# Kernel tuning notes

Measured on AMD Instinct MI355X. Metric: run time of the kernel, lower is better.

The kernel has to match this reference:

```python
import jax, jax.numpy as jnp
import numpy as np

N, E, F_IN, H, C_OUT, G, L = 50000, 400000, 128, 128, 10, 512, 3
EPS = 1e-5
BN_BIAS = 1e-4  # BatchNorm1d weights init to 1, biases to 1e-4 in the source


def batchnorm(x):
    # training-mode BN, gamma=1, beta=1e-4 (as initialized in the module)
    m = x.mean(0)
    v = jnp.mean((x - m) ** 2, 0)
    return (x - m) * jax.lax.rsqrt(v + EPS) + BN_BIAS


def gcn_conv(x, W, b, src, dst, edge_weight=None):
    """CAL-style GCNConv: x@W, add self loops (weight 1), sym deg^-1/2 norm, scatter-add to dst."""
    n = x.shape[0]
    h = x @ W
    ew = jnp.ones(src.shape[0], x.dtype) if edge_weight is None else edge_weight
    loop = jnp.arange(n)
    row = jnp.concatenate([src, loop])
    col = jnp.concatenate([dst, loop])
    ew = jnp.concatenate([ew, jnp.ones(n, x.dtype)])
    deg = jax.ops.segment_sum(ew, row, num_segments=n)
    dis = jax.lax.rsqrt(jnp.where(deg > 0, deg, 1.0)) * (deg > 0)
    norm = dis[row] * ew * dis[col]
    out = jax.ops.segment_sum(norm[:, None] * h[row], col, num_segments=n)
    return out + b


def setup_inputs():
    key = jax.random.key(0)
    ks = jax.random.split(key, 32)
    rn = lambda k, shp, s=0.1: jax.random.normal(k, shp, jnp.float32) * s
    src = jax.random.randint(ks[0], (E,), 0, N, jnp.int32)
    dst = jax.random.randint(ks[1], (E,), 0, N, jnp.int32)
    dst = jnp.where(dst == src, (dst + 1) % N, dst)  # no self loops in data edges
    batch = jnp.sort(jax.random.randint(ks[2], (N,), 0, G, jnp.int32))
    return {
        'x': jax.random.normal(ks[3], (N, F_IN), jnp.float32),
        'W_feat': rn(ks[4], (F_IN, H)),
        'conv_Ws': rn(ks[5], (L, H, H)), 'conv_bs': rn(ks[6], (L, H), 0.01),
        'eW': rn(ks[7], (2 * H, 2)), 'eb': rn(ks[8], (2,), 0.01),
        'naW': rn(ks[9], (H, 2)), 'nab': rn(ks[10], (2,), 0.01),
        'xcW': rn(ks[11], (H, H)), 'xcb': rn(ks[12], (H,), 0.01),
        'xoW': rn(ks[13], (H, H)), 'xob': rn(ks[14], (H,), 0.01),
        'cW1': rn(ks[15], (H, H)), 'cb1': rn(ks[16], (H,), 0.01),
        'cW2': rn(ks[17], (H, C_OUT)), 'cb2': rn(ks[18], (C_OUT,), 0.01),
        'oW1': rn(ks[19], (H, H)), 'ob1': rn(ks[20], (H,), 0.01),
        'oW2': rn(ks[21], (H, C_OUT)), 'ob2': rn(ks[22], (C_OUT,), 0.01),
        'coW1': rn(ks[23], (2 * H, H)), 'cob1': rn(ks[24], (H,), 0.01),
        'coW2': rn(ks[25], (H, C_OUT)), 'cob2': rn(ks[26], (C_OUT,), 0.01),
        'edge_src': src, 'edge_dst': dst, 'batch': batch,
    }


def _forward(x, W_feat, conv_Ws, conv_bs, eW, eb, naW, nab, xcW, xcb, xoW, xob,
             cW1, cb1, cW2, cb2, oW1, ob1, oW2, ob2, coW1, cob1, coW2, cob2,
             edge_src, edge_dst, batch):
    # BIG: BN -> gfn conv (linear, no bias, no propagate) -> [BN -> GCNConv -> relu] x L
    h = batchnorm(x)
    h = jax.nn.relu(h @ W_feat)
    for i in range(L):
        h = batchnorm(h)
        h = jax.nn.relu(gcn_conv(h, conv_Ws[i], conv_bs[i], edge_src, edge_dst))
    # Att_cov: per-edge MLP softmax + per-node GCNConv softmax (shared by XC/XO)
    edge_rep = jnp.concatenate([h[edge_src], h[edge_dst]], axis=-1)  # [E, 2H]
    edge_att = jax.nn.softmax(edge_rep @ eW + eb, axis=-1)           # [E, 2]
    node_att = jax.nn.softmax(gcn_conv(h, naW, nab, edge_src, edge_dst), axis=-1)  # [N, 2]
    # XC branch (channel 0)
    xc = node_att[:, 0:1] * h
    xc = jax.nn.elu(gcn_conv(batchnorm(xc), xcW, xcb, edge_src, edge_dst, edge_att[:, 0]))
    xc = jax.ops.segment_sum(xc, batch, num_segments=G)  # global_add_pool [G, H]
    # XO branch (channel 1)
    xo = node_att[:, 1:2] * h
    xo = jax.nn.elu(gcn_conv(batchnorm(xo), xoW, xob, edge_src, edge_dst, edge_att[:, 1]))
    xo = jax.ops.segment_sum(xo, batch, num_segments=G)
    # C head
    c = batchnorm(xc)
    c = jax.nn.relu(c @ cW1 + cb1)
    c = batchnorm(c)
    c = jax.nn.log_softmax(c @ cW2 + cb2, axis=-1)
    # O head (Dropout1d inactive in eval)
    o = batchnorm(xo)
    o = jax.nn.relu(o @ oW1 + ob1)
    o = batchnorm(o)
    o = jax.nn.log_softmax(o @ oW2 + ob2, axis=-1)
    # CO head (cat branch; eval_random=False -> identity permutation); note elu applied twice
    co = jnp.concatenate([xc, xo], axis=1)
    co = batchnorm(co)
    co = jax.nn.elu(jax.nn.elu(co @ coW1 + cob1))
    co = batchnorm(co)
    co = jax.nn.log_softmax(co @ coW2 + cob2, axis=-1)
    return c, o, co


def reference(x, W_feat, conv_Ws, conv_bs, eW, eb, naW, nab, xcW, xcb, xoW, xob,
              cW1, cb1, cW2, cb2, oW1, ob1, oW2, ob2, coW1, cob1, coW2, cob2,
              edge_src, edge_dst, batch):
    return _forward(x, W_feat, conv_Ws, conv_bs, eW, eb, naW, nab, xcW, xcb, xoW, xob,
                    cW1, cb1, cW2, cb2, oW1, ob1, oW2, ob2, coW1, cob1, coW2, cob2,
                    edge_src, edge_dst, batch)
```

## Files before the change

### kernel.cpp

```cpp
#include <hip/hip_runtime.h>


typedef unsigned short bf16_t;
typedef unsigned int   uint32;
typedef __attribute__((ext_vector_type(8))) short   bf16x8;
typedef __attribute__((ext_vector_type(4))) float   f32x4;

__device__ __forceinline__ float b2f(bf16_t v){ return __uint_as_float(((uint32)v) << 16); }
__device__ __forceinline__ bf16_t f2b(float f){
    uint32 u = __float_as_uint(f);
    return (bf16_t)((u + 0x7fffu + ((u >> 16) & 1u)) >> 16);
}
__device__ __forceinline__ uint32 pack2(float lo, float hi){
    return (uint32)f2b(lo) | ((uint32)f2b(hi) << 16);
}
__device__ __forceinline__ float lo16(uint32 u){ return __uint_as_float(u << 16); }
__device__ __forceinline__ float hi16(uint32 u){ return __uint_as_float(u & 0xffff0000u); }
__device__ __forceinline__ int   rl (int v, int l){ return __builtin_amdgcn_readlane(v, l); }
__device__ __forceinline__ float rlf(float v, int l){
    return __int_as_float(__builtin_amdgcn_readlane(__float_as_int(v), l));
}

__global__ void k_prologue(const float* __restrict__ Wf, const float* __restrict__ cWs,
        const float* __restrict__ xcW, const float* __restrict__ xoW,
        bf16_t* __restrict__ whiT, bf16_t* __restrict__ wloT,
        const int* __restrict__ esrc, const int* __restrict__ edst,
        int* __restrict__ cnt, float* __restrict__ degU, int* __restrict__ rankE, int e,
        const float* __restrict__ x, float* __restrict__ st, int n, int gridE)
{
    __shared__ float red[2][8][128];
    int bx = blockIdx.x, tid = threadIdx.x;
    if (bx < 96){
        int mat = bx >> 4, sub = bx & 15;
        const float* src = (mat == 0) ? Wf : (mat <= 3) ? cWs + (size_t)(mat - 1) * 16384
                          : (mat == 4) ? xcW : xoW;
        int i = (sub * 256 + tid) * 4;
        int nrow = i >> 7, k0 = i & 127;
        size_t off = (size_t)mat * 16384 + (size_t)nrow * 128 + k0;
        #pragma unroll
        for (int j = 0; j < 4; ++j){
            float w = src[(size_t)(k0 + j) * 128 + nrow];
            bf16_t h = f2b(w);
            whiT[off + j] = h;
            wloT[off + j] = f2b(w - b2f(h));
        }
    } else if (bx < 96 + gridE){
        int i = (bx - 96) * 256 + tid;
        if (i < e){
            int r = atomicAdd(&cnt[edst[i]], 1);
            rankE[i] = r;
            atomicAdd(&degU[esrc[i]], 1.0f);
        }
    } else {
        int bb = bx - 96 - gridE;
        int f4 = (tid & 31) * 4, slice = tid >> 5;
        float s[4] = {0,0,0,0}, q[4] = {0,0,0,0};
        for (int row = bb * 8 + slice; row < n; row += 2048){
            float4 v = *(const float4*)&x[(size_t)row * 128 + f4];
            s[0]+=v.x; q[0]+=v.x*v.x; s[1]+=v.y; q[1]+=v.y*v.y;
            s[2]+=v.z; q[2]+=v.z*v.z; s[3]+=v.w; q[3]+=v.w*v.w;
        }
        #pragma unroll
        for (int j = 0; j < 4; ++j){ red[0][slice][f4+j]=s[j]; red[1][slice][f4+j]=q[j]; }
        __syncthreads();
        if (tid < 128){
            float ts=0.f, tq=0.f;
            #pragma unroll
            for (int w = 0; w < 8; ++w){ ts += red[0][w][tid]; tq += red[1][w][tid]; }
            atomicAdd(&st[tid], ts); atomicAdd(&st[128+tid], tq);
        }
    }
}

__global__ __launch_bounds__(256) void k_statsB(const bf16_t* __restrict__ a,
        float* __restrict__ st, int n){
    __shared__ float red[2][16][128];
    int tid = threadIdx.x;
    int c8 = (tid & 15) * 8, slice = tid >> 4;
    float s[8] = {0,0,0,0,0,0,0,0}, q[8] = {0,0,0,0,0,0,0,0};
    for (int row = blockIdx.x * 16 + slice; row < n; row += 4096){
        uint4 v = *(const uint4*)&a[(size_t)row * 128 + c8];
        const bf16_t* pv = (const bf16_t*)&v;
        #pragma unroll
        for (int j = 0; j < 8; ++j){ float f = b2f(pv[j]); s[j] += f; q[j] += f * f; }
    }
    #pragma unroll
    for (int j = 0; j < 8; ++j){ red[0][slice][c8+j]=s[j]; red[1][slice][c8+j]=q[j]; }
    __syncthreads();
    if (tid < 128){
        float ts=0.f, tq=0.f;
        #pragma unroll
        for (int w = 0; w < 16; ++w){ ts += red[0][w][tid]; tq += red[1][w][tid]; }
        atomicAdd(&st[tid], ts); atomicAdd(&st[128+tid], tq);
    }
}

template<int ACT, int INBF>
__global__ __launch_bounds__(256, 3) void k_gemm(const void* __restrict__ Av,
        const float* __restrict__ scale, int sch,
        const float* __restrict__ st, const bf16_t* __restrict__ WhiT,
        const bf16_t* __restrict__ WloT,
        bf16_t* __restrict__ C, int ldc, int ccol0, int n)
{
    __shared__ bf16_t As[64 * 136];
    __shared__ bf16_t Whi[128 * 72];
    __shared__ bf16_t Wlo[128 * 72];
    int tid = threadIdx.x;
    int wid = tid >> 6, lane = tid & 63;
    int row0 = blockIdx.x * 64;
    int m0 = wid * 16;
    int q8 = (lane >> 4) * 8, l15 = lane & 15;

    int c8t = (tid & 15) * 8;
    float sM[8], sR[8];
    #pragma unroll
    for (int j = 0; j < 8; ++j){
        float m = st[c8t + j] / n;
        float var = st[128 + c8t + j] / n - m * m;
        sM[j] = m; sR[j] = rsqrtf(var + 1e-5f);
    }

    for (int i = tid; i < 64 * 16; i += 256){
        int r = i >> 4, c8 = (i & 15) * 8;
        int gr = row0 + r;
        float v[8];
        if (gr < n){
            float sc = scale ? scale[(size_t)gr * 2 + sch] : 1.f;
            if (INBF){
                const bf16_t* Ab = (const bf16_t*)Av;
                ushort4 qa = *(const ushort4*)&Ab[(size_t)gr * 128 + c8];
                ushort4 qb = *(const ushort4*)&Ab[(size_t)gr * 128 + c8 + 4];
                v[0]=b2f(qa.x); v[1]=b2f(qa.y); v[2]=b2f(qa.z); v[3]=b2f(qa.w);
                v[4]=b2f(qb.x); v[5]=b2f(qb.y); v[6]=b2f(qb.z); v[7]=b2f(qb.w);
            } else {
                const float* Af = (const float*)Av;
                float4 fa = *(const float4*)&Af[(size_t)gr * 128 + c8];
                float4 fb = *(const float4*)&Af[(size_t)gr * 128 + c8 + 4];
                v[0]=fa.x; v[1]=fa.y; v[2]=fa.z; v[3]=fa.w;
                v[4]=fb.x; v[5]=fb.y; v[6]=fb.z; v[7]=fb.w;
            }
            #pragma unroll
            for (int j = 0; j < 8; ++j)
                v[j] = (v[j] * sc - sM[j]) * sR[j] + 1e-4f;
        } else {
            #pragma unroll
            for (int j = 0; j < 8; ++j) v[j] = 0.f;
        }
        #pragma unroll
        for (int j = 0; j < 8; ++j) As[r * 136 + c8 + j] = f2b(v[j]);
    }

    f32x4 acc[8];
    #pragma unroll
    for (int t = 0; t < 8; ++t) acc[t] = (f32x4){0.f, 0.f, 0.f, 0.f};

    for (int kc = 0; kc < 128; kc += 64){
        __syncthreads();
        for (int i = tid; i < 128 * 8; i += 256){
            int nrow = i >> 3, k8 = (i & 7) * 8;
            *(uint4*)&Whi[nrow * 72 + k8] = *(const uint4*)&WhiT[(size_t)nrow * 128 + kc + k8];
            *(uint4*)&Wlo[nrow * 72 + k8] = *(const uint4*)&WloT[(size_t)nrow * 128 + kc + k8];
        }
        __syncthreads();
        #pragma unroll
        for (int kbl = 0; kbl < 2; ++kbl){
            bf16x8 a = *(const bf16x8*)&As[(m0 + l15) * 136 + kc + kbl * 32 + q8];
            #pragma unroll
            for (int nt = 0; nt < 8; ++nt){
                bf16x8 bh = *(const bf16x8*)&Whi[(nt * 16 + l15) * 72 + kbl * 32 + q8];
                acc[nt] = __builtin_amdgcn_mfma_f32_16x16x32_bf16(a, bh, acc[nt], 0, 0, 0);
                bf16x8 bl = *(const bf16x8*)&Wlo[(nt * 16 + l15) * 72 + kbl * 32 + q8];
                acc[nt] = __builtin_amdgcn_mfma_f32_16x16x32_bf16(a, bl, acc[nt], 0, 0, 0);
            }
        }
    }

    __syncthreads();
    #pragma unroll
    for (int nt = 0; nt < 8; ++nt){
        #pragma unroll
        for (int r = 0; r < 4; ++r){
            float v = acc[nt][r];
            if (ACT == 1) v = fmaxf(v, 0.f);
            As[(m0 + (lane >> 4) * 4 + r) * 136 + nt * 16 + l15] = f2b(v);
        }
    }
    __syncthreads();
    for (int i = tid; i < 64 * 16; i += 256){
        int r = i >> 4, c8 = (i & 15) * 8;
        int gr = row0 + r;
        if (gr < n)
            *(uint4*)&C[(size_t)gr * ldc + ccol0 + c8] = *(const uint4*)&As[r * 136 + c8];
    }
}

__global__ __launch_bounds__(256, 3) void k_gemm2(const bf16_t* __restrict__ Ab,
        const float* __restrict__ natt, const float* __restrict__ stBase,
        const bf16_t* __restrict__ whiT6, const bf16_t* __restrict__ wloT6,
        bf16_t* __restrict__ C, int n)
{
    __shared__ bf16_t As[64 * 136];
    __shared__ bf16_t Whi[128 * 72];
    __shared__ bf16_t Wlo[128 * 72];
    int brn = blockIdx.y;
    const float* st = stBase + brn * 256;
    const bf16_t* WhiT = whiT6 + (size_t)(4 + brn) * 16384;
    const bf16_t* WloT = wloT6 + (size_t)(4 + brn) * 16384;
    int ccol0 = brn * 128;
    const int ldc = 256;

    int tid = threadIdx.x;
    int wid = tid >> 6, lane = tid & 63;
    int row0 = blockIdx.x * 64;
    int m0 = wid * 16;
    int q8 = (lane >> 4) * 8, l15 = lane & 15;

    int c8t = (tid & 15) * 8;
    float sM[8], sR[8];
    #pragma unroll
    for (int j = 0; j < 8; ++j){
        float m = st[c8t + j] / n;
        float var = st[128 + c8t + j] / n - m * m;
        sM[j] = m; sR[j] = rsqrtf(var + 1e-5f);
    }

    for (int i = tid; i < 64 * 16; i += 256){
        int r = i >> 4, c8 = (i & 15) * 8;
        int gr = row0 + r;
        float v[8];
        if (gr < n){
            float sc = natt[(size_t)gr * 2 + brn];
            ushort4 qa = *(const ushort4*)&Ab[(size_t)gr * 128 + c8];
            ushort4 qb = *(const ushort4*)&Ab[(size_t)gr * 128 + c8 + 4];
            v[0]=b2f(qa.x); v[1]=b2f(qa.y); v[2]=b2f(qa.z); v[3]=b2f(qa.w);
            v[4]=b2f(qb.x); v[5]=b2f(qb.y); v[6]=b2f(qb.z); v[7]=b2f(qb.w);
            #pragma unroll
            for (int j = 0; j < 8; ++j)
                v[j] = (v[j] * sc - sM[j]) * sR[j] + 1e-4f;
        } else {
            #pragma unroll
            for (int j = 0; j < 8; ++j) v[j] = 0.f;
        }
        #pragma unroll
        for (int j = 0; j < 8; ++j) As[r * 136 + c8 + j] = f2b(v[j]);
    }

    f32x4 acc[8];
    #pragma unroll
    for (int t = 0; t < 8; ++t) acc[t] = (f32x4){0.f, 0.f, 0.f, 0.f};

    for (int kc = 0; kc < 128; kc += 64){
        __syncthreads();
        for (int i = tid; i < 128 * 8; i += 256){
            int nrow = i >> 3, k8 = (i & 7) * 8;
            *(uint4*)&Whi[nrow * 72 + k8] = *(const uint4*)&WhiT[(size_t)nrow * 128 + kc + k8];
            *(uint4*)&Wlo[nrow * 72 + k8] = *(const uint4*)&WloT[(size_t)nrow * 128 + kc + k8];
        }
        __syncthreads();
        #pragma unroll
        for (int kbl = 0; kbl < 2; ++kbl){
            bf16x8 a = *(const bf16x8*)&As[(m0 + l15) * 136 + kc + kbl * 32 + q8];
            #pragma unroll
            for (int nt = 0; nt < 8; ++nt){
                bf16x8 bh = *(const bf16x8*)&Whi[(nt * 16 + l15) * 72 + kbl * 32 + q8];
                acc[nt] = __builtin_amdgcn_mfma_f32_16x16x32_bf16(a, bh, acc[nt], 0, 0, 0);
                bf16x8 bl = *(const bf16x8*)&Wlo[(nt * 16 + l15) * 72 + kbl * 32 + q8];
                acc[nt] = __builtin_amdgcn_mfma_f32_16x16x32_bf16(a, bl, acc[nt], 0, 0, 0);
            }
        }
    }

    __syncthreads();
    #pragma unroll
    for (int nt = 0; nt < 8; ++nt){
        #pragma unroll
        for (int r = 0; r < 4; ++r){
            As[(m0 + (lane >> 4) * 4 + r) * 136 + nt * 16 + l15] = f2b(acc[nt][r]);
        }
    }
    __syncthreads();
    for (int i = tid; i < 64 * 16; i += 256){
        int r = i >> 4, c8 = (i & 15) * 8;
        int gr = row0 + r;
        if (gr < n)
            *(uint4*)&C[(size_t)gr * ldc + ccol0 + c8] = *(const uint4*)&As[r * 136 + c8];
    }
}

__global__ __launch_bounds__(1024) void k_scanA(const int* __restrict__ cnt,
        int* __restrict__ ptr, int* __restrict__ bsum, int n){
    __shared__ int wsum[16];
    int t = threadIdx.x, lane = t & 63, wid = t >> 6;
    int i = blockIdx.x * 1024 + t;
    int v = (i < n) ? cnt[i] : 0;
    int s = v;
    for (int off = 1; off < 64; off <<= 1){
        int u = __shfl_up(s, off);
        if (lane >= off) s += u;
    }
    if (lane == 63) wsum[wid] = s;
    __syncthreads();
    if (wid == 0 && lane < 16){
        int ws = wsum[lane];
        for (int off = 1; off < 16; off <<= 1){
            int u = __shfl_up(ws, off);
            if (lane >= off) ws += u;
        }
        wsum[lane] = ws;
    }
    __syncthreads();
    int woff = wid ? wsum[wid - 1] : 0;
    if (i < n) ptr[i] = woff + s - v;
    if (t == 1023) bsum[blockIdx.x] = woff + s;
}
__global__ void k_scanB(int* __restrict__ bsum, int* __restrict__ ptrN, int nb){
    int lane = threadIdx.x;
    int carry = 0;
    for (int base = 0; base < nb; base += 64){
        int i = base + lane;
        int v = (i < nb) ? bsum[i] : 0;
        int s = v;
        for (int off = 1; off < 64; off <<= 1){
            int u = __shfl_up(s, off);
            if (lane >= off) s += u;
        }
        if (i < nb) bsum[i] = carry + s - v;
        carry += __shfl(s, 63);
    }
    if (lane == 0) *ptrN = carry;
}
__global__ __launch_bounds__(1024) void k_scanC(int* __restrict__ ptr,
        const int* __restrict__ bsum, int n){
    int i = blockIdx.x * 1024 + threadIdx.x;
    if (i < n) ptr[i] += bsum[blockIdx.x];
}
__global__ void k_fill(const int* __restrict__ src, const int* __restrict__ dst,
                       const int* __restrict__ rankE, const int* __restrict__ ptr,
                       int* __restrict__ srcC, int* __restrict__ dstC,
                       const float* __restrict__ degU, float* __restrict__ wU, int e){
    int i = blockIdx.x * 256 + threadIdx.x;
    if (i < e){
        int s = src[i];
        int d = dst[i];
        int slot = ptr[d] + rankE[i];
        srcC[slot] = s;
        dstC[slot] = d;
        wU[slot] = rsqrtf(degU[s] + 1.0f);
    }
}

template<int PREP>
__global__ __launch_bounds__(256) void k_gather0(const int* __restrict__ ptr,
        const int* __restrict__ srcC, const float* __restrict__ wE,
        const float* __restrict__ degU, const bf16_t* __restrict__ t,
        const float* __restrict__ bias, bf16_t* __restrict__ outB,
        const float* __restrict__ eW, const float* __restrict__ naW,
        float4* __restrict__ epre, float* __restrict__ ntT, int n)
{
    int node = blockIdx.x * 4 + (threadIdx.x >> 6);
    if (node >= n) return;
    int lane = threadIdx.x & 63;
    const uint32* T = (const uint32*)t;
    float dd = rsqrtf(degU[node] + 1.0f);
    uint32 sv = T[(size_t)node * 64 + lane];
    float a0 = 0.f, a1 = 0.f;
    int k = ptr[node], end = ptr[node + 1];
    while (k < end){
        int cnt = min(end - k, 64);
        int kl = k + min(lane, cnt - 1);
        int   myI = srcC[kl];
        float myW = wE[kl];
        int j = 0;
        for (; j + 8 <= cnt; j += 8){
            int s0 = rl(myI, j),     s1 = rl(myI, j + 1), s2 = rl(myI, j + 2), s3 = rl(myI, j + 3);
            int s4 = rl(myI, j + 4), s5 = rl(myI, j + 5), s6 = rl(myI, j + 6), s7 = rl(myI, j + 7);
            float w0 = rlf(myW, j),     w1 = rlf(myW, j + 1), w2 = rlf(myW, j + 2), w3 = rlf(myW, j + 3);
            float w4 = rlf(myW, j + 4), w5 = rlf(myW, j + 5), w6 = rlf(myW, j + 6), w7 = rlf(myW, j + 7);
            uint32 v0 = T[(size_t)s0 * 64 + lane];
            uint32 v1 = T[(size_t)s1 * 64 + lane];
            uint32 v2 = T[(size_t)s2 * 64 + lane];
            uint32 v3 = T[(size_t)s3 * 64 + lane];
            uint32 v4 = T[(size_t)s4 * 64 + lane];
            uint32 v5 = T[(size_t)s5 * 64 + lane];
            uint32 v6 = T[(size_t)s6 * 64 + lane];
            uint32 v7 = T[(size_t)s7 * 64 + lane];
            a0 += w0 * lo16(v0) + w1 * lo16(v1) + w2 * lo16(v2) + w3 * lo16(v3);
            a1 += w0 * hi16(v0) + w1 * hi16(v1) + w2 * hi16(v2) + w3 * hi16(v3);
            a0 += w4 * lo16(v4) + w5 * lo16(v5) + w6 * lo16(v6) + w7 * lo16(v7);
            a1 += w4 * hi16(v4) + w5 * hi16(v5) + w6 * hi16(v6) + w7 * hi16(v7);
        }
        for (; j < cnt; ++j){
            int s = rl(myI, j);
            float w = rlf(myW, j);
            uint32 v = T[(size_t)s * 64 + lane];
            a0 += w * lo16(v); a1 += w * hi16(v);
        }
        k += cnt;
    }
    a0 = fmaxf(dd * (a0 + dd * lo16(sv)) + bias[2 * lane],     0.f);
    a1 = fmaxf(dd * (a1 + dd * hi16(sv)) + bias[2 * lane + 1], 0.f);
    ((uint32*)outB)[(size_t)node * 64 + lane] = pack2(a0, a1);
    if (PREP){
        float s0 = a0 * eW[4 * lane]           + a1 * eW[4 * lane + 2];
        float s1 = a0 * eW[4 * lane + 1]       + a1 * eW[4 * lane + 3];
        float d0 = a0 * eW[256 + 4 * lane]     + a1 * eW[256 + 4 * lane + 2];
        float d1 = a0 * eW[256 + 4 * lane + 1] + a1 * eW[256 + 4 * lane + 3];
        float n0 = a0 * naW[4 * lane]          + a1 * naW[4 * lane + 2];
        float n1 = a0 * naW[4 * lane + 1]      + a1 * naW[4 * lane + 3];
        for (int off = 32; off; off >>= 1){
            s0 += __shfl_xor(s0, off); s1 += __shfl_xor(s1, off);
            d0 += __shfl_xor(d0, off); d1 += __shfl_xor(d1, off);
            n0 += __shfl_xor(n0, off); n1 += __shfl_xor(n1, off);
        }
        if (lane == 0){
            epre[node] = make_float4(s0, s1, d0, d1);
            ntT[2 * node] = n0; ntT[2 * node + 1] = n1;
        }
    }
}

__global__ __launch_bounds__(256) void k_gatherP2(const int* __restrict__ ptr,
        const int* __restrict__ srcC, const float* __restrict__ w0E,
        const float* __restrict__ w1E, const float* __restrict__ degC0,
        const float* __restrict__ degU, const bf16_t* __restrict__ t,
        const float* __restrict__ biasC, const float* __restrict__ biasO,
        const int* __restrict__ batch, float* __restrict__ pool0,
        float* __restrict__ pool1, int n, int span)
{
    int br   = blockIdx.x & 1;
    int wave = (blockIdx.x >> 1) * 4 + (threadIdx.x >> 6);
    int lane = threadIdx.x & 63;
    int nbeg = wave * span;
    if (nbeg >= n) return;
    int nend = min(n, nbeg + span);
    const float* wE   = br ? w1E : w0E;
    const float* bias = br ? biasO : biasC;
    float* pool       = br ? pool1 : pool0;
    float b0 = bias[2 * lane], b1 = bias[2 * lane + 1];
    const uint32* T = (const uint32*)t;
    int rowoff = (br ? 64 : 0) + lane;
    int curG = -1;
    float p0 = 0.f, p1 = 0.f;
    for (int node = nbeg; node < nend; ++node){
        float d0v = degC0[node];
        float dv  = br ? (degU[node] - d0v) : d0v;
        float dd  = rsqrtf(dv + 1.0f);
        uint32 sv = T[(size_t)node * 128 + rowoff];
        float a0 = 0.f, a1 = 0.f;
        int k = ptr[node], end = ptr[node + 1];
        while (k < end){
            int cnt = min(end - k, 64);
            int kl = k + min(lane, cnt - 1);
            int   myI = srcC[kl];
            float myW = wE[kl];
            int j = 0;
            for (; j + 8 <= cnt; j += 8){
                int s0 = rl(myI, j),     s1 = rl(myI, j + 1), s2 = rl(myI, j + 2), s3 = rl(myI, j + 3);
                int s4 = rl(myI, j + 4), s5 = rl(myI, j + 5), s6 = rl(myI, j + 6), s7 = rl(myI, j + 7);
                float w0 = rlf(myW, j),     w1 = rlf(myW, j + 1), w2 = rlf(myW, j + 2), w3 = rlf(myW, j + 3);
                float w4 = rlf(myW, j + 4), w5 = rlf(myW, j + 5), w6 = rlf(myW, j + 6), w7 = rlf(myW, j + 7);
                uint32 v0 = T[(size_t)s0 * 128 + rowoff];
                uint32 v1 = T[(size_t)s1 * 128 + rowoff];
                uint32 v2 = T[(size_t)s2 * 128 + rowoff];
                uint32 v3 = T[(size_t)s3 * 128 + rowoff];
                uint32 v4 = T[(size_t)s4 * 128 + rowoff];
                uint32 v5 = T[(size_t)s5 * 128 + rowoff];
                uint32 v6 = T[(size_t)s6 * 128 + rowoff];
                uint32 v7 = T[(size_t)s7 * 128 + rowoff];
                a0 += w0 * lo16(v0) + w1 * lo16(v1) + w2 * lo16(v2) + w3 * lo16(v3);
                a1 += w0 * hi16(v0) + w1 * hi16(v1) + w2 * hi16(v2) + w3 * hi16(v3);
                a0 += w4 * lo16(v4) + w5 * lo16(v5) + w6 * lo16(v6) + w7 * lo16(v7);
                a1 += w4 * hi16(v4) + w5 * hi16(v5) + w6 * hi16(v6) + w7 * hi16(v7);
            }
            for (; j < cnt; ++j){
                int s = rl(myI, j);
                float w = rlf(myW, j);
                uint32 v = T[(size_t)s * 128 + rowoff];
                a0 += w * lo16(v); a1 += w * hi16(v);
            }
            k += cnt;
        }
        a0 = dd * (a0 + dd * lo16(sv)) + b0;
        a1 = dd * (a1 + dd * hi16(sv)) + b1;
        a0 = a0 > 0.f ? a0 : expm1f(a0);
        a1 = a1 > 0.f ? a1 : expm1f(a1);
        int g = batch[node];
        if (g != curG){
            if (curG >= 0){
                float* p = pool + (size_t)curG * 128 + 2 * lane;
                atomicAdd(&p[0], p0); atomicAdd(&p[1], p1);
            }
            curG = g; p0 = a0; p1 = a1;
        } else {
            p0 += a0; p1 += a1;
        }
    }
    if (curG >= 0){
        float* p = pool + (size_t)curG * 128 + 2 * lane;
        atomicAdd(&p[0], p0); atomicAdd(&p[1], p1);
    }
}

__global__ void k_eattnatt(const int* __restrict__ srcC, const int* __restrict__ dstC,
        const float4* __restrict__ epre, const float* __restrict__ eb,
        float* __restrict__ wB0, float* __restrict__ wB1,
        float* __restrict__ d0,
        const int* __restrict__ ptr, const float* __restrict__ wU,
        const float* __restrict__ degU, const float* __restrict__ ntT,
        const float* __restrict__ nab, float* __restrict__ natt,
        int e, int n, int gridN)
{
    int bx = blockIdx.x;
    if (bx < gridN){
        int i = bx * 256 + threadIdx.x;
        if (i >= n) return;
        float dd = rsqrtf(degU[i] + 1.0f);
        float z0 = 0.f, z1 = 0.f;
        int end = ptr[i + 1];
        for (int k = ptr[i]; k < end; ++k){
            int s = srcC[k];
            float w = wU[k];
            z0 += w * ntT[2 * s]; z1 += w * ntT[2 * s + 1];
        }
        z0 = dd * (z0 + dd * ntT[2 * i])     + nab[0];
        z1 = dd * (z1 + dd * ntT[2 * i + 1]) + nab[1];
        float m = fmaxf(z0, z1);
        float e0 = expf(z0 - m), e1 = expf(z1 - m);
        float inv = 1.f / (e0 + e1);
        natt[2 * i] = e0 * inv; natt[2 * i + 1] = e1 * inv;
    } else {
        int i = (bx - gridN) * 256 + threadIdx.x;
        if (i >= e) return;
        int s = srcC[i];
        float4 ps = epre[s], pd = epre[dstC[i]];
        float l0 = ps.x + pd.z + eb[0], l1 = ps.y + pd.w + eb[1];
        float m = fmaxf(l0, l1);
        float e0 = expf(l0 - m), e1 = expf(l1 - m);
        float inv = 1.f / (e0 + e1);
        e0 *= inv; e1 *= inv;
        wB0[i] = e0; wB1[i] = e1;
        atomicAdd(&d0[s], e0);
    }
}

__global__ void k_stats2wB(const bf16_t* __restrict__ a, const float* __restrict__ natt,
        float* __restrict__ st, int n,
        const int* __restrict__ srcC, const float* __restrict__ degC0,
        const float* __restrict__ degU, float* __restrict__ w0,
        float* __restrict__ w1, int e)
{
    __shared__ float red[2][16][128];
    int bx = blockIdx.x, tid = threadIdx.x;
    if (bx < 256){
        int c8 = (tid & 15) * 8, slice = tid >> 4;
        float s0[8]={0,0,0,0,0,0,0,0}, q0[8]={0,0,0,0,0,0,0,0};
        float s1[8]={0,0,0,0,0,0,0,0}, q1[8]={0,0,0,0,0,0,0,0};
        for (int row = bx * 16 + slice; row < n; row += 4096){
            uint4 v = *(const uint4*)&a[(size_t)row * 128 + c8];
            const bf16_t* pv = (const bf16_t*)&v;
            float2 w = *(const float2*)&natt[(size_t)row * 2];
            #pragma unroll
            for (int j = 0; j < 8; ++j){
                float f = b2f(pv[j]);
                float f0 = f * w.x, f1 = f * w.y;
                s0[j] += f0; q0[j] += f0 * f0;
                s1[j] += f1; q1[j] += f1 * f1;
            }
        }
        #pragma unroll
        for (int j = 0; j < 8; ++j){ red[0][slice][c8+j]=s0[j]; red[1][slice][c8+j]=q0[j]; }
        __syncthreads();
        if (tid < 128){
            float ts=0.f, tq=0.f;
            #pragma unroll
            for (int w = 0; w < 16; ++w){ ts += red[0][w][tid]; tq += red[1][w][tid]; }
            atomicAdd(&st[tid], ts); atomicAdd(&st[128+tid], tq);
        }
        __syncthreads();
        #pragma unroll
        for (int j = 0; j < 8; ++j){ red[0][slice][c8+j]=s1[j]; red[1][slice][c8+j]=q1[j]; }
        __syncthreads();
        if (tid < 128){
            float ts=0.f, tq=0.f;
            #pragma unroll
            for (int w = 0; w < 16; ++w){ ts += red[0][w][tid]; tq += red[1][w][tid]; }
            atomicAdd(&st[256+tid], ts); atomicAdd(&st[384+tid], tq);
        }
    } else {
        int i = (bx - 256) * 256 + tid;
        if (i < e){
            int s = srcC[i];
            float d0v = degC0[s];
            w0[i] *= rsqrtf(d0v + 1.0f);
            w1[i] *= rsqrtf(degU[s] - d0v + 1.0f);
        }
    }
}

__global__ __launch_bounds__(1024) void k_gstats3(const float* __restrict__ xcp,
        const float* __restrict__ xop, float* __restrict__ mrsH, int n){
    __shared__ float red[2][1024];
    int head = blockIdx.x;
    const float* a = (head == 1) ? xop : xcp;
    const float* b = (head == 0) ? xcp : xop;
    int f = (head == 2) ? 256 : 128;
    float* mrs = mrsH + head * 512;
    int col = threadIdx.x & (f - 1);
    int rpb = 1024 / f;
    int rw  = threadIdx.x / f;
    float s = 0.f, sq = 0.f;
    for (int r = rw; r < n; r += rpb){
        float v = (col < 128) ? a[(size_t)r * 128 + col] : b[(size_t)r * 128 + col - 128];
        s += v; sq += v * v;
    }
    red[0][threadIdx.x] = s; red[1][threadIdx.x] = sq;
    __syncthreads();
    if (threadIdx.x < (unsigned)f){
        float ts = 0.f, tq = 0.f;
        for (int w = 0; w < rpb; ++w){ ts += red[0][w * f + col]; tq += red[1][w * f + col]; }
        float m = ts / n, var = tq / n - m * m;
        mrs[col] = m; mrs[f + col] = rsqrtf(var + 1e-5f);
    }
}
__global__ __launch_bounds__(128) void k_hgemm3(const float* __restrict__ xcp,
        const float* __restrict__ xop, const float* __restrict__ mrsH,
        const float* __restrict__ cW1, const float* __restrict__ cb1,
        const float* __restrict__ oW1, const float* __restrict__ ob1,
        const float* __restrict__ coW1, const float* __restrict__ cob1,
        float* __restrict__ gt3)
{
    __shared__ float as[256];
    int head = blockIdx.y, row = blockIdx.x, tid = threadIdx.x;
    const float* a  = (head == 1) ? xop : xcp;
    const float* b2 = (head == 0) ? xcp : xop;
    int fin = (head == 2) ? 256 : 128;
    const float* mrs = mrsH + head * 512;
    const float* W  = (head == 0) ? cW1 : (head == 1) ? oW1 : coW1;
    const float* bb = (head == 0) ? cb1 : (head == 1) ? ob1 : cob1;
    float* o = gt3 + (size_t)head * 512 * 128;
    for (int i = tid; i < fin; i += 128){
        float v = (i < 128) ? a[(size_t)row * 128 + i] : b2[(size_t)row * 128 + i - 128];
        as[i] = (v - mrs[i]) * mrs[fin + i] + 1e-4f;
    }
    __syncthreads();
    float s = 0.f;
    for (int k = 0; k < fin; ++k) s += as[k] * W[k * 128 + tid];
    s += bb[tid];
    if (head < 2) s = fmaxf(s, 0.f);
    else { s = s > 0.f ? s : expm1f(s); s = s > 0.f ? s : expm1f(s); }
    o[(size_t)row * 128 + tid] = s;
}
__global__ __launch_bounds__(1024) void k_gstats3b(const float* __restrict__ gt3,
        float* __restrict__ mrsH2, int n){
    __shared__ float red[2][1024];
    int head = blockIdx.x;
    const float* a = gt3 + (size_t)head * 512 * 128;
    float* mrs = mrsH2 + head * 256;
    int col = threadIdx.x & 127;
    int rw  = threadIdx.x >> 7;
    float s = 0.f, sq = 0.f;
    for (int r = rw; r < n; r += 8){
        float v = a[(size_t)r * 128 + col];
        s += v; sq += v * v;
    }
    red[0][threadIdx.x] = s; red[1][threadIdx.x] = sq;
    __syncthreads();
    if (threadIdx.x < 128u){
        float ts = 0.f, tq = 0.f;
        for (int w = 0; w < 8; ++w){ ts += red[0][w * 128 + col]; tq += red[1][w * 128 + col]; }
        float m = ts / n, var = tq / n - m * m;
        mrs[col] = m; mrs[128 + col] = rsqrtf(var + 1e-5f);
    }
}
__global__ __launch_bounds__(256) void k_hfinal3(const float* __restrict__ gt3,
        const float* __restrict__ mrsH2,
        const float* __restrict__ cW2, const float* __restrict__ cb2,
        const float* __restrict__ oW2, const float* __restrict__ ob2,
        const float* __restrict__ coW2, const float* __restrict__ cob2,
        float* __restrict__ out, int nrows)
{
    int head = blockIdx.y;
    int row = blockIdx.x * 4 + (threadIdx.x >> 6);
    if (row >= nrows) return;
    int lane = threadIdx.x & 63;
    const float* a   = gt3 + (size_t)head * 512 * 128;
    const float* mrs = mrsH2 + head * 256;
    const float* W = (head == 0) ? cW2 : (head == 1) ? oW2 : coW2;
    const float* b = (head == 0) ? cb2 : (head == 1) ? ob2 : cob2;
    float* o = out + (size_t)head * nrows * 10;
    float v0 = (a[(size_t)row * 128 + lane]      - mrs[lane])      * mrs[128 + lane]      + 1e-4f;
    float v1 = (a[(size_t)row * 128 + 64 + lane] - mrs[64 + lane]) * mrs[128 + 64 + lane] + 1e-4f;
    float logit[10];
    #pragma unroll
    for (int c = 0; c < 10; ++c){
        float p = v0 * W[lane * 10 + c] + v1 * W[(lane + 64) * 10 + c];
        for (int off = 32; off; off >>= 1) p += __shfl_xor(p, off);
        logit[c] = p + b[c];
    }
    float m = logit[0];
    #pragma unroll
    for (int c = 1; c < 10; ++c) m = fmaxf(m, logit[c]);
    float s = 0.f;
    #pragma unroll
    for (int c = 0; c < 10; ++c) s += expf(logit[c] - m);
    float lse = logf(s);
    if (lane < 10) o[row * 10 + lane] = logit[lane] - m - lse;
}

extern "C" void kernel_launch(void* const* d_in, const int* in_sizes, int n_in,
                              void* d_out, int out_size, void* d_ws, size_t ws_size,
                              hipStream_t stream)
{
    const int N = in_sizes[0] / 128;
    const int E = in_sizes[24];
    const int G = 512;
    const float* x    = (const float*)d_in[0];
    const float* Wf   = (const float*)d_in[1];
    const float* cWs  = (const float*)d_in[2];
    const float* cbs  = (const float*)d_in[3];
    const float* eW   = (const float*)d_in[4];
    const float* ebv  = (const float*)d_in[5];
    const float* naW  = (const float*)d_in[6];
    const float* nab  = (const float*)d_in[7];
    const float* xcW  = (const float*)d_in[8];
    const float* xcb  = (const float*)d_in[9];
    const float* xoW  = (const float*)d_in[10];
    const float* xob  = (const float*)d_in[11];
    const float* cW1  = (const float*)d_in[12];
    const float* cb1  = (const float*)d_in[13];
    const float* cW2  = (const float*)d_in[14];
    const float* cb2  = (const float*)d_in[15];
    const float* oW1  = (const float*)d_in[16];
    const float* ob1  = (const float*)d_in[17];
    const float* oW2  = (const float*)d_in[18];
    const float* ob2  = (const float*)d_in[19];
    const float* coW1 = (const float*)d_in[20];
    const float* cob1 = (const float*)d_in[21];
    const float* coW2 = (const float*)d_in[22];
    const float* cob2 = (const float*)d_in[23];
    const int* esrc  = (const int*)d_in[24];
    const int* edst  = (const int*)d_in[25];
    const int* batch = (const int*)d_in[26];
    float* out = (float*)d_out;

    size_t NH = (size_t)N * 128;
    bf16_t* B1  = (bf16_t*)d_ws;
    bf16_t* B0  = B1 + NH;
    bf16_t* B0c = B0 + NH;
    float* fbase = (float*)(B0c + 2 * NH);
    float* epreF = fbase;
    float* ntT   = epreF + 4 * (size_t)N;
    float* natt  = ntT + 2 * (size_t)N;
    float* mrsH  = natt + 2 * (size_t)N;
    float* mrsH2 = mrsH + 1536;
    float* wU    = mrsH2 + 768;
    float* wB0   = wU + E;
    float* wB1   = wB0 + E;
    float* gt3   = wB1 + E;
    float* zz    = gt3 + (size_t)3 * G * 128;
    float* degU  = zz;
    float* degC0 = degU + N;
    float* degC1 = degC0 + N;
    float* stZ   = degC1 + N;
    float* xcp   = stZ + 1536;
    float* xop   = xcp + (size_t)G * 128;
    int*   cntI  = (int*)(xop + (size_t)G * 128);
    size_t zzBytes = ((size_t)(4 * N) + 1536 + 2 * (size_t)G * 128) * 4;
    int* ptrI   = cntI + N;
    int* srcC   = ptrI + N + 1;
    int* dstC   = srcC + E;
    int* bsum   = dstC + E;
    int* rankE  = bsum + 64;
    bf16_t* whiT = (bf16_t*)((((size_t)(rankE + E)) + 15) & ~(size_t)15);
    bf16_t* wloT = whiT + 6 * 16384;
    float4* epre = (float4*)epreF;

    int gridE = (E + 255) / 256;
    int gridN = (N + 255) / 256;
    int gridW = (N + 3) / 4;
    int gridG = (N + 63) / 64;
    int nb    = (N + 1023) / 1024;
    int span  = (N + 16383) / 16384;
    int gridP = (N + span * 4 - 1) / (span * 4);

    hipMemsetAsync(zz, 0, zzBytes, stream);

    k_prologue<<<96 + gridE + 256, 256, 0, stream>>>(Wf, cWs, xcW, xoW, whiT, wloT,
            esrc, edst, cntI, degU, rankE, E, x, stZ, N, gridE);

    k_scanA<<<nb, 1024, 0, stream>>>(cntI, ptrI, bsum, N);
    k_scanB<<<1, 64, 0, stream>>>(bsum, ptrI + N, nb);
    k_scanC<<<nb, 1024, 0, stream>>>(ptrI, bsum, N);
    k_fill<<<gridE, 256, 0, stream>>>(esrc, edst, rankE, ptrI, srcC, dstC, degU, wU, E);

    k_gemm<1, 0><<<gridG, 256, 0, stream>>>(x, nullptr, 0, stZ, whiT, wloT, B1, 128, 0, N);

    for (int i = 0; i < 3; ++i){
        float* st = stZ + 256 * (i + 1);
        k_statsB<<<256, 256, 0, stream>>>(B1, st, N);
        k_gemm<0, 1><<<gridG, 256, 0, stream>>>(B1, nullptr, 0, st,
                whiT + (size_t)(i + 1) * 16384, wloT + (size_t)(i + 1) * 16384,
                B0, 128, 0, N);
        if (i < 2)
            k_gather0<0><<<gridW, 256, 0, stream>>>(ptrI, srcC, wU, degU, B0,
                    cbs + i * 128, B1, eW, naW, epre, ntT, N);
        else
            k_gather0<1><<<gridW, 256, 0, stream>>>(ptrI, srcC, wU, degU, B0,
                    cbs + i * 128, B1, eW, naW, epre, ntT, N);
    }

    k_eattnatt<<<gridN + gridE, 256, 0, stream>>>(srcC, dstC, epre, ebv, wB0, wB1,
            degC0, ptrI, wU, degU, ntT, nab, natt, E, N, gridN);

    k_stats2wB<<<256 + gridE, 256, 0, stream>>>(B1, natt, stZ + 1024, N,
            srcC, degC0, degU, wB0, wB1, E);

    k_gemm2<<<dim3(gridG, 2), 256, 0, stream>>>(B1, natt, stZ + 1024, whiT, wloT, B0c, N);
    k_gatherP2<<<2 * gridP, 256, 0, stream>>>(ptrI, srcC, wB0, wB1, degC0, degU, B0c,
                                              xcb, xob, batch, xcp, xop, N, span);

    k_gstats3<<<3, 1024, 0, stream>>>(xcp, xop, mrsH, G);
    k_hgemm3<<<dim3(G, 3), 128, 0, stream>>>(xcp, xop, mrsH, cW1, cb1, oW1, ob1,
                                             coW1, cob1, gt3);
    k_gstats3b<<<3, 1024, 0, stream>>>(gt3, mrsH2, G);
    k_hfinal3<<<dim3((G + 3) / 4, 3), 256, 0, stream>>>(gt3, mrsH2, cW2, cb2, oW2, ob2,
                                                        coW2, cob2, out, G);
}
```

Baseline: 574.8 us.

## Replace global atomic CSR build with chunked LDS histograms and add source-sorted CSR

Edge counting now uses per-chunk packed 16-bit shared-memory histograms over 64 edge chunks instead of global atomics per edge. A chunk-prefix scan pass turns these into per-chunk offsets, which give a deterministic fill of both a destination-sorted and a new source-sorted CSR. The edge-attention source degree (degC0) is then computed as a per-source gather over the source CSR instead of global float atomics, and the large memset shrinks. In exchange it adds a chunk-scan kernel, a doubled prefix scan, extra rank and offset tables, and recomputes the edge softmax during that gather.

```diff
diff --git a/kernel.cpp b/kernel.cpp
--- a/kernel.cpp
+++ b/kernel.cpp
@@ -5,6 +5,8 @@
 typedef unsigned int   uint32;
 typedef __attribute__((ext_vector_type(8))) short   bf16x8;
 typedef __attribute__((ext_vector_type(4))) float   f32x4;
+
+#define CHNK 64
 
 __device__ __forceinline__ float b2f(bf16_t v){ return __uint_as_float(((uint32)v) << 16); }
 __device__ __forceinline__ bf16_t f2b(float f){
@@ -25,13 +27,43 @@
         const float* __restrict__ xcW, const float* __restrict__ xoW,
         bf16_t* __restrict__ whiT, bf16_t* __restrict__ wloT,
         const int* __restrict__ esrc, const int* __restrict__ edst,
-        int* __restrict__ cnt, float* __restrict__ degU, int* __restrict__ rankE, int e,
-        const float* __restrict__ x, float* __restrict__ st, int n, int gridE)
-{
-    __shared__ float red[2][8][128];
+        uint32* __restrict__ cntD16, uint32* __restrict__ cntS16,
+        int* __restrict__ rankE, int* __restrict__ rankS, int e,
+        const float* __restrict__ x, float* __restrict__ st, int n, int WD)
+{
+    __shared__ uint32 h[12544];
     int bx = blockIdx.x, tid = threadIdx.x;
-    if (bx < 96){
-        int mat = bx >> 4, sub = bx & 15;
+    if (bx < 256){
+        int side = bx >> 7;
+        int sub = bx & 127;
+        int c = sub >> 1, hh = sub & 1;
+        int Nh = ((n + 3) / 4) * 2;
+        int lo = hh ? Nh : 0;
+        int hi = hh ? n : Nh;
+        int w0 = lo >> 1;
+        int nw = (hi - lo + 1) >> 1;
+        for (int j = tid; j < nw; j += 256) h[j] = 0;
+        __syncthreads();
+        int EC = (e + CHNK - 1) / CHNK;
+        int beg = c * EC, endE = min(e, beg + EC);
+        const int* keys = side ? esrc : edst;
+        int* rank = side ? rankS : rankE;
+        for (int i = beg + tid; i < endE; i += 256){
+            int d = keys[i];
+            if (d >= lo && d < hi){
+                int w = (d >> 1) - w0;
+                int sh = (d & 1) * 16;
+                uint32 old = atomicAdd(&h[w], 1u << sh);
+                rank[i] = (int)((old >> sh) & 0xffffu);
+            }
+        }
+        __syncthreads();
+        uint32* table = side ? cntS16 : cntD16;
+        for (int j = tid; j < nw; j += 256)
+            table[(size_t)c * WD + w0 + j] = h[j];
+    } else if (bx < 352){
+        int ms = bx - 256;
+        int mat = ms >> 4, sub = ms & 15;
         const float* src = (mat == 0) ? Wf : (mat <= 3) ? cWs + (size_t)(mat - 1) * 16384
                           : (mat == 4) ? xcW : xoW;
         int i = (sub * 256 + tid) * 4;
@@ -40,19 +72,13 @@
         #pragma unroll
         for (int j = 0; j < 4; ++j){
             float w = src[(size_t)(k0 + j) * 128 + nrow];
-            bf16_t h = f2b(w);
-            whiT[off + j] = h;
-            wloT[off + j] = f2b(w - b2f(h));
-        }
-    } else if (bx < 96 + gridE){
-        int i = (bx - 96) * 256 + tid;
-        if (i < e){
-            int r = atomicAdd(&cnt[edst[i]], 1);
-            rankE[i] = r;
-            atomicAdd(&degU[esrc[i]], 1.0f);
+            bf16_t hb = f2b(w);
+            whiT[off + j] = hb;
+            wloT[off + j] = f2b(w - b2f(hb));
         }
     } else {
-        int bb = bx - 96 - gridE;
+        int bb = bx - 352;
+        float* red = (float*)h;
         int f4 = (tid & 31) * 4, slice = tid >> 5;
         float s[4] = {0,0,0,0}, q[4] = {0,0,0,0};
         for (int row = bb * 8 + slice; row < n; row += 2048){
@@ -61,14 +87,42 @@
             s[2]+=v.z; q[2]+=v.z*v.z; s[3]+=v.w; q[3]+=v.w*v.w;
         }
         #pragma unroll
-        for (int j = 0; j < 4; ++j){ red[0][slice][f4+j]=s[j]; red[1][slice][f4+j]=q[j]; }
+        for (int j = 0; j < 4; ++j){
+            red[slice * 128 + f4 + j] = s[j];
+            red[1024 + slice * 128 + f4 + j] = q[j];
+        }
         __syncthreads();
         if (tid < 128){
             float ts=0.f, tq=0.f;
             #pragma unroll
-            for (int w = 0; w < 8; ++w){ ts += red[0][w][tid]; tq += red[1][w][tid]; }
+            for (int w = 0; w < 8; ++w){ ts += red[w*128+tid]; tq += red[1024+w*128+tid]; }
             atomicAdd(&st[tid], ts); atomicAdd(&st[128+tid], tq);
         }
+    }
+}
+
+__global__ void k_chunkscan(uint32* __restrict__ cntD16, uint32* __restrict__ cntS16,
+        int* __restrict__ cntI, float* __restrict__ degUf, int WD, int n)
+{
+    int g = blockIdx.x * 256 + threadIdx.x;
+    if (g >= 2 * WD) return;
+    int side = (g >= WD);
+    int w = side ? g - WD : g;
+    uint32* tab = side ? cntS16 : cntD16;
+    uint32 r0 = 0, r1 = 0;
+    for (int c = 0; c < CHNK; ++c){
+        size_t idx = (size_t)c * WD + w;
+        uint32 v = tab[idx];
+        tab[idx] = r0 | (r1 << 16);
+        r0 += v & 0xffffu; r1 += v >> 16;
+    }
+    int b0 = 2 * w, b1 = 2 * w + 1;
+    if (!side){
+        if (b0 < n) cntI[b0] = (int)r0;
+        if (b1 < n) cntI[b1] = (int)r1;
+    } else {
+        if (b0 < n){ cntI[n + b0] = (int)r0; degUf[b0] = (float)r0; }
+        if (b1 < n){ cntI[n + b1] = (int)r1; degUf[b1] = (float)r1; }
     }
 }
 
@@ -334,19 +388,27 @@
     int i = blockIdx.x * 1024 + threadIdx.x;
     if (i < n) ptr[i] += bsum[blockIdx.x];
 }
-__global__ void k_fill(const int* __restrict__ src, const int* __restrict__ dst,
-                       const int* __restrict__ rankE, const int* __restrict__ ptr,
-                       int* __restrict__ srcC, int* __restrict__ dstC,
-                       const float* __restrict__ degU, float* __restrict__ wU, int e){
+__global__ void k_fill(const int* __restrict__ esrc, const int* __restrict__ edst,
+        const int* __restrict__ rankE, const int* __restrict__ rankS,
+        const uint32* __restrict__ cntD16, const uint32* __restrict__ cntS16,
+        const int* __restrict__ ptr, const float* __restrict__ degUf,
+        int* __restrict__ srcC, int* __restrict__ dstC, int* __restrict__ dstS,
+        float* __restrict__ wU, int e, int n, int WD, int EC)
+{
     int i = blockIdx.x * 256 + threadIdx.x;
-    if (i < e){
-        int s = src[i];
-        int d = dst[i];
-        int slot = ptr[d] + rankE[i];
-        srcC[slot] = s;
-        dstC[slot] = d;
-        wU[slot] = rsqrtf(degU[s] + 1.0f);
-    }
+    if (i >= e) return;
+    int s = esrc[i], d = edst[i];
+    int c = i / EC;
+    uint32 pw = cntD16[(size_t)c * WD + (d >> 1)];
+    int offD = (d & 1) ? (int)(pw >> 16) : (int)(pw & 0xffffu);
+    int dslot = ptr[d] + offD + rankE[i];
+    uint32 sw = cntS16[(size_t)c * WD + (s >> 1)];
+    int offS = (s & 1) ? (int)(sw >> 16) : (int)(sw & 0xffffu);
+    int sslot = (ptr[n + s] - e) + offS + rankS[i];
+    srcC[dslot] = s;
+    dstC[dslot] = d;
+    wU[dslot] = rsqrtf(degUf[s] + 1.0f);
+    dstS[sslot] = d;
 }
 
 template<int PREP>
@@ -502,13 +564,14 @@
 }
 
 __global__ void k_eattnatt(const int* __restrict__ srcC, const int* __restrict__ dstC,
+        const int* __restrict__ dstS,
         const float4* __restrict__ epre, const float* __restrict__ eb,
         float* __restrict__ wB0, float* __restrict__ wB1,
-        float* __restrict__ d0,
+        float* __restrict__ degC0,
         const int* __restrict__ ptr, const float* __restrict__ wU,
         const float* __restrict__ degU, const float* __restrict__ ntT,
         const float* __restrict__ nab, float* __restrict__ natt,
-        int e, int n, int gridN)
+        int e, int n, int gridN, int gridE)
 {
     int bx = blockIdx.x;
     if (bx < gridN){
@@ -528,7 +591,7 @@
         float e0 = expf(z0 - m), e1 = expf(z1 - m);
         float inv = 1.f / (e0 + e1);
         natt[2 * i] = e0 * inv; natt[2 * i + 1] = e1 * inv;
-    } else {
+    } else if (bx < gridN + gridE){
         int i = (bx - gridN) * 256 + threadIdx.x;
         if (i >= e) return;
         int s = srcC[i];
@@ -537,9 +600,23 @@
         float m = fmaxf(l0, l1);
         float e0 = expf(l0 - m), e1 = expf(l1 - m);
         float inv = 1.f / (e0 + e1);
-        e0 *= inv; e1 *= inv;
-        wB0[i] = e0; wB1[i] = e1;
-        atomicAdd(&d0[s], e0);
+        wB0[i] = e0 * inv; wB1[i] = e1 * inv;
+    } else {
+        int s = (bx - gridN - gridE) * 256 + threadIdx.x;
+        if (s >= n) return;
+        float4 ps = epre[s];
+        float eb0 = eb[0], eb1 = eb[1];
+        int beg = ptr[n + s] - e, endk = ptr[n + s + 1] - e;
+        float sum = 0.f;
+        for (int k = beg; k < endk; ++k){
+            int d = dstS[k];
+            float4 pd = epre[d];
+            float l0 = ps.x + pd.z + eb0, l1 = ps.y + pd.w + eb1;
+            float m = fmaxf(l0, l1);
+            float e0 = expf(l0 - m), e1v = expf(l1 - m);
+            sum += e0 / (e0 + e1v);
+        }
+        degC0[s] = sum;
     }
 }
 
@@ -743,6 +820,9 @@
     const int* batch = (const int*)d_in[26];
     float* out = (float*)d_out;
 
+    const int WD = (N + 1) / 2;
+    const int EC = (E + CHNK - 1) / CHNK;
+
     size_t NH = (size_t)N * 128;
     bf16_t* B1  = (bf16_t*)d_ws;
     bf16_t* B0  = B1 + NH;
@@ -757,21 +837,23 @@
     float* wB0   = wU + E;
     float* wB1   = wB0 + E;
     float* gt3   = wB1 + E;
-    float* zz    = gt3 + (size_t)3 * G * 128;
-    float* degU  = zz;
+    float* degU  = gt3 + (size_t)3 * G * 128;
     float* degC0 = degU + N;
-    float* degC1 = degC0 + N;
-    float* stZ   = degC1 + N;
+    float* stZ   = degC0 + N;
     float* xcp   = stZ + 1536;
     float* xop   = xcp + (size_t)G * 128;
-    int*   cntI  = (int*)(xop + (size_t)G * 128);
-    size_t zzBytes = ((size_t)(4 * N) + 1536 + 2 * (size_t)G * 128) * 4;
-    int* ptrI   = cntI + N;
-    int* srcC   = ptrI + N + 1;
+    size_t zzBytes = (1536 + 2 * (size_t)G * 128) * 4;
+    int* cntI   = (int*)(xop + (size_t)G * 128);
+    int* ptrI   = cntI + 2 * N;
+    int* srcC   = ptrI + 2 * N + 1;
     int* dstC   = srcC + E;
-    int* bsum   = dstC + E;
-    int* rankE  = bsum + 64;
-    bf16_t* whiT = (bf16_t*)((((size_t)(rankE + E)) + 15) & ~(size_t)15);
+    int* dstS   = dstC + E;
+    int* rankE  = dstS + E;
+    int* rankS  = rankE + E;
+    int* bsum   = rankS + E;
+    uint32* cntD16 = (uint32*)(bsum + 128);
+    uint32* cntS16 = cntD16 + (size_t)CHNK * WD;
+    bf16_t* whiT = (bf16_t*)((((size_t)(cntS16 + (size_t)CHNK * WD)) + 15) & ~(size_t)15);
     bf16_t* wloT = whiT + 6 * 16384;
     float4* epre = (float4*)epreF;
 
@@ -779,19 +861,23 @@
     int gridN = (N + 255) / 256;
     int gridW = (N + 3) / 4;
     int gridG = (N + 63) / 64;
-    int nb    = (N + 1023) / 1024;
+    int n2    = 2 * N;
+    int nb2   = (n2 + 1023) / 1024;
+    int gridCS = (2 * WD + 255) / 256;
     int span  = (N + 16383) / 16384;
     int gridP = (N + span * 4 - 1) / (span * 4);
 
-    hipMemsetAsync(zz, 0, zzBytes, stream);
-
-    k_prologue<<<96 + gridE + 256, 256, 0, stream>>>(Wf, cWs, xcW, xoW, whiT, wloT,
-            esrc, edst, cntI, degU, rankE, E, x, stZ, N, gridE);
-
-    k_scanA<<<nb, 1024, 0, stream>>>(cntI, ptrI, bsum, N);
-    k_scanB<<<1, 64, 0, stream>>>(bsum, ptrI + N, nb);
-    k_scanC<<<nb, 1024, 0, stream>>>(ptrI, bsum, N);
-    k_fill<<<gridE, 256, 0, stream>>>(esrc, edst, rankE, ptrI, srcC, dstC, degU, wU, E);
+    hipMemsetAsync(stZ, 0, zzBytes, stream);
+
+    k_prologue<<<608, 256, 0, stream>>>(Wf, cWs, xcW, xoW, whiT, wloT,
+            esrc, edst, cntD16, cntS16, rankE, rankS, E, x, stZ, N, WD);
+
+    k_chunkscan<<<gridCS, 256, 0, stream>>>(cntD16, cntS16, cntI, degU, WD, N);
+    k_scanA<<<nb2, 1024, 0, stream>>>(cntI, ptrI, bsum, n2);
+    k_scanB<<<1, 64, 0, stream>>>(bsum, ptrI + n2, nb2);
+    k_scanC<<<nb2, 1024, 0, stream>>>(ptrI, bsum, n2);
+    k_fill<<<gridE, 256, 0, stream>>>(esrc, edst, rankE, rankS, cntD16, cntS16,
+            ptrI, degU, srcC, dstC, dstS, wU, E, N, WD, EC);
 
     k_gemm<1, 0><<<gridG, 256, 0, stream>>>(x, nullptr, 0, stZ, whiT, wloT, B1, 128, 0, N);
 
@@ -809,8 +895,8 @@
                     cbs + i * 128, B1, eW, naW, epre, ntT, N);
     }
 
-    k_eattnatt<<<gridN + gridE, 256, 0, stream>>>(srcC, dstC, epre, ebv, wB0, wB1,
-            degC0, ptrI, wU, degU, ntT, nab, natt, E, N, gridN);
+    k_eattnatt<<<gridN + gridE + gridN, 256, 0, stream>>>(srcC, dstC, dstS, epre, ebv,
+            wB0, wB1, degC0, ptrI, wU, degU, ntT, nab, natt, E, N, gridN, gridE);
 
     k_stats2wB<<<256 + gridE, 256, 0, stream>>>(B1, natt, stZ + 1024, N,
             srcC, degC0, degU, wB0, wB1, E);
```

Result: faster. 558.4 us (-2.9%).
